# Kernel optimization log

Hardware: AMD Instinct MI355X
Metric: run time of the kernel (lower is better)

The kernel has to match this reference:

```python
import jax, jax.numpy as jnp
import numpy as np

B, N, H, T = 128, 512, 128, 32


def setup_inputs() -> dict:
    key = jax.random.key(0)
    ks = jax.random.split(key, 6)
    s = 0.05  # small init scale keeps softmax logits sane
    return {
        "encoder_outputs": jax.random.normal(ks[0], (B, N, H), jnp.float32),
        "W_ih": jax.random.normal(ks[1], (4 * H, H), jnp.float32) * s,
        "W_hh": jax.random.normal(ks[2], (4 * H, H), jnp.float32) * s,
        "b_ih": jnp.zeros((4 * H,), jnp.float32),
        "b_hh": jnp.zeros((4 * H,), jnp.float32),
        "W1": jax.random.normal(ks[3], (H, H), jnp.float32) * s,
        "W2": jax.random.normal(ks[4], (H, H), jnp.float32) * s,
        "v": jax.random.normal(ks[5], (H,), jnp.float32) * s,
        "decode_steps": T,
    }


def reference(encoder_outputs, W_ih, W_hh, b_ih, b_hh, W1, W2, v, decode_steps):
    b, n, h = encoder_outputs.shape
    dtype = encoder_outputs.dtype
    # W1(encoder_outputs) is loop-invariant: hoist it (same math as the torch loop)
    enc_trans = jnp.einsum("bnh,kh->bnk", encoder_outputs, W1)  # [B,n,H]

    dec0 = encoder_outputs.mean(axis=1)  # [B,H]
    hx0 = jnp.zeros((b, h), dtype)
    cx0 = jnp.zeros((b, h), dtype)
    mask0 = jnp.zeros((b, n), bool)
    key0 = jax.random.key(42)
    rows = jnp.arange(b)

    def step(carry, _):
        dec_input, hx, cx, mask, key = carry
        # torch.nn.LSTMCell: gates ordered i, f, g, o
        gates = dec_input @ W_ih.T + b_ih + hx @ W_hh.T + b_hh  # [B,4H]
        i, f, g, o = jnp.split(gates, 4, axis=-1)
        i = jax.nn.sigmoid(i)
        f = jax.nn.sigmoid(f)
        g = jnp.tanh(g)
        o = jax.nn.sigmoid(o)
        cx_new = f * cx + i * g
        hx_new = o * jnp.tanh(cx_new)
        # additive attention scores
        dec_trans = hx_new @ W2.T  # [B,H]
        scores = jnp.einsum("bnh,h->bn", jnp.tanh(enc_trans + dec_trans[:, None, :]), v)
        scores = jnp.where(mask, -jnp.inf, scores)  # masked_fill(-inf)
        # sample next node (torch.multinomial on softmax == categorical on logits)
        key, sub = jax.random.split(key)
        idx = jax.random.categorical(sub, scores, axis=-1)  # [B]
        probs = jax.nn.softmax(scores, axis=-1)
        sel_log_prob = jnp.log(jnp.take_along_axis(probs, idx[:, None], axis=1)[:, 0] + 1e-9)
        mask_new = mask.at[rows, idx].set(True)
        dec_next = jnp.take_along_axis(encoder_outputs, idx[:, None, None], axis=1)[:, 0]  # [B,H]
        return (dec_next, hx_new, cx_new, mask_new, key), (idx, sel_log_prob)

    _, (tours, log_probs) = jax.lax.scan(
        step, (dec0, hx0, cx0, mask0, key0), xs=None, length=decode_steps
    )
    return tours.T, log_probs.T  # [B,T], [B,T]
```

## Files before the change

### kernel.cpp

```cpp
#include <hip/hip_runtime.h>
#include <cstdint>
#include <cstddef>


constexpr int B = 128, N = 512, H = 128, T = 32;
constexpr int G4 = 4 * H;
constexpr float TINYF = 1.17549435e-38f;

__host__ __device__ inline uint32_t rotl32(uint32_t v, int d) {
  return (v << d) | (v >> (32 - d));
}

__host__ __device__ inline void tf2x32(uint32_t k0, uint32_t k1,
                                       uint32_t x0, uint32_t x1,
                                       uint32_t& o0, uint32_t& o1) {
  uint32_t ks2 = k0 ^ k1 ^ 0x1BD11BDAu;
  x0 += k0; x1 += k1;
#define TF_R(r) x0 += x1; x1 = rotl32(x1, (r)); x1 ^= x0;
  TF_R(13) TF_R(15) TF_R(26) TF_R(6)
  x0 += k1; x1 += ks2 + 1u;
  TF_R(17) TF_R(29) TF_R(16) TF_R(24)
  x0 += ks2; x1 += k0 + 2u;
  TF_R(13) TF_R(15) TF_R(26) TF_R(6)
  x0 += k0; x1 += k1 + 3u;
  TF_R(17) TF_R(29) TF_R(16) TF_R(24)
  x0 += k1; x1 += ks2 + 4u;
  TF_R(13) TF_R(15) TF_R(26) TF_R(6)
  x0 += ks2; x1 += k0 + 5u;
#undef TF_R
  o0 = x0; o1 = x1;
}

struct KeyArgs { uint32_t k[2 * T]; };

static KeyArgs make_subkeys() {
  KeyArgs ka;
  uint32_t k0 = 0u, k1 = 42u;
  for (int t = 0; t < T; ++t) {
    uint32_t n0, n1, s0, s1;
    tf2x32(k0, k1, 0u, 0u, n0, n1);
    tf2x32(k0, k1, 0u, 1u, s0, s1);
    ka.k[2 * t] = s0; ka.k[2 * t + 1] = s1;
    k0 = n0; k1 = n1;
  }
  return ka;
}

__device__ inline uint32_t gumbel_bits(uint32_t sk0, uint32_t sk1, int i) {
  uint32_t o0, o1;
  tf2x32(sk0, sk1, 0u, (uint32_t)i, o0, o1);
  return o0 ^ o1;
}

__device__ inline float fast_tanh(float x) {
  float cx = fminf(9.0f, fmaxf(-9.0f, x));
  float t = __expf(2.0f * cx);
  return (t - 1.0f) * __builtin_amdgcn_rcpf(t + 1.0f);
}

__global__ void k_transpose(const float* __restrict__ Wih, const float* __restrict__ Whh,
                            const float* __restrict__ W2, const float* __restrict__ W1,
                            float* __restrict__ WihT, float* __restrict__ WhhT,
                            float* __restrict__ W2T, float* __restrict__ W1T) {
  int i = blockIdx.x * blockDim.x + threadIdx.x;
  if (i < H * G4) {
    int h = i >> 9, j = i & (G4 - 1);
    WihT[i] = Wih[j * H + h];
  } else if (i < 2 * H * G4) {
    int q = i - H * G4; int h = q >> 9, j = q & (G4 - 1);
    WhhT[q] = Whh[j * H + h];
  } else if (i < 2 * H * G4 + H * H) {
    int q = i - 2 * H * G4; int h = q >> 7, k = q & (H - 1);
    W2T[q] = W2[k * H + h];
  } else if (i < 2 * H * G4 + 2 * H * H) {
    int q = i - 2 * H * G4 - H * H; int h = q >> 7, k = q & (H - 1);
    W1T[q] = W1[k * H + h];
  }
}

__global__ __launch_bounds__(256) void k_enc_trans(const float* __restrict__ enc,
                                                   const float* __restrict__ W1T,
                                                   float* __restrict__ encT2) {
  __shared__ __align__(16) float es[16 * 128];
  int blk = blockIdx.x;
  int b = blk >> 5;
  int n0 = (blk & 31) << 4;
  const float* src = enc + ((size_t)b * N + n0) * H;
  for (int i = threadIdx.x; i < 16 * 128; i += 256) es[i] = src[i];
  __syncthreads();
  int k = threadIdx.x & 127, ng = threadIdx.x >> 7;
  float acc[8] = {0.f, 0.f, 0.f, 0.f, 0.f, 0.f, 0.f, 0.f};
  for (int h = 0; h < H; h += 4) {
    float w0 = W1T[(h + 0) * H + k];
    float w1 = W1T[(h + 1) * H + k];
    float w2 = W1T[(h + 2) * H + k];
    float w3 = W1T[(h + 3) * H + k];
#pragma unroll
    for (int j = 0; j < 8; ++j) {
      const float4 e = *(const float4*)&es[(ng * 8 + j) * 128 + h];
      acc[j] += w0 * e.x + w1 * e.y + w2 * e.z + w3 * e.w;
    }
  }
  float* dst = encT2 + (size_t)b * H * N + (size_t)k * N + n0 + ng * 8;
  ((float4*)dst)[0] = make_float4(acc[0], acc[1], acc[2], acc[3]);
  ((float4*)dst)[1] = make_float4(acc[4], acc[5], acc[6], acc[7]);
}

__global__ __launch_bounds__(1024) void k_decode(
    const float* __restrict__ enc, const float* __restrict__ encT2,
    const float* __restrict__ WihT, const float* __restrict__ WhhT,
    const float* __restrict__ W2T,
    const float* __restrict__ bih, const float* __restrict__ bhh,
    const float* __restrict__ v,
    KeyArgs keys, float* __restrict__ out) {
  __shared__ __align__(16) float xs[H];
  __shared__ __align__(16) float hs[H];
  __shared__ __align__(16) float cs[H];
  __shared__ __align__(16) float dt[H];
  __shared__ __align__(16) float vv[H];
  __shared__ __align__(16) float bsum[G4];
  __shared__ float pg[2][G4];
  __shared__ float ps[2][N];
  __shared__ float pdt[4][H];
  __shared__ float sc[N];
  __shared__ float wr_z[8], wr_m[8], wr_s[8];
  __shared__ int wr_i[8];
  __shared__ float s_smax;
  __shared__ int s_idx;

  const int tid = threadIdx.x;
  const int b = blockIdx.x;
  const int lane = tid & 63;
  const int wave = tid >> 6;
  const int half = tid >> 9;
  const int id = tid & 511;

  if (tid < 512) {
    int h = tid & 127, part = tid >> 7;
    float s = 0.f;
    const float* p = enc + ((size_t)b * N + part * 128) * H + h;
#pragma unroll 8
    for (int n = 0; n < 128; ++n) s += p[(size_t)n * H];
    pdt[part][h] = s;
    bsum[tid] = bih[tid] + bhh[tid];
  }
  if (tid < 128) { hs[tid] = 0.f; cs[tid] = 0.f; vv[tid] = v[tid]; }
  __syncthreads();
  if (tid < 128)
    xs[tid] = (pdt[0][tid] + pdt[1][tid] + pdt[2][tid] + pdt[3][tid]) * (1.0f / N);
  bool masked = false;
  __syncthreads();

  for (int t = 0; t < T; ++t) {
    {
      const float* wi = WihT + (size_t)(half * 64) * G4 + id;
      const float* wh = WhhT + (size_t)(half * 64) * G4 + id;
      const int hb = half * 64;
      float a0 = 0.f, a1 = 0.f;
#pragma unroll 8
      for (int h = 0; h < 64; ++h) {
        a0 += wi[h * G4] * xs[hb + h];
        a1 += wh[h * G4] * hs[hb + h];
      }
      pg[half][id] = a0 + a1;
    }
    __syncthreads();
    if (tid < 128) {
      float gi = pg[0][tid] + pg[1][tid] + bsum[tid];
      float gf = pg[0][H + tid] + pg[1][H + tid] + bsum[H + tid];
      float gg = pg[0][2 * H + tid] + pg[1][2 * H + tid] + bsum[2 * H + tid];
      float go = pg[0][3 * H + tid] + pg[1][3 * H + tid] + bsum[3 * H + tid];
      gi = 1.0f / (1.0f + expf(-gi));
      gf = 1.0f / (1.0f + expf(-gf));
      gg = tanhf(gg);
      go = 1.0f / (1.0f + expf(-go));
      float c = gf * cs[tid] + gi * gg;
      cs[tid] = c;
      hs[tid] = go * tanhf(c);
    }
    __syncthreads();
    if (tid < 512) {
      int k = tid & 127, part = tid >> 7;
      const float* w2 = W2T + (size_t)(part * 32) * H + k;
      const int hb = part * 32;
      float a = 0.f;
#pragma unroll 8
      for (int h = 0; h < 32; ++h) a += w2[h * H] * hs[hb + h];
      pdt[part][k] = a;
    }
    __syncthreads();
    if (tid < 128) dt[tid] = pdt[0][tid] + pdt[1][tid] + pdt[2][tid] + pdt[3][tid];
    __syncthreads();
    {
      const int kb = half * 64;
      const float* ep = encT2 + (size_t)b * (H * N) + (size_t)kb * N + id;
      float a0 = 0.f, a1 = 0.f;
#pragma unroll 8
      for (int kk = 0; kk < 64; kk += 2) {
        float e0 = ep[(size_t)kk * N];
        float e1 = ep[(size_t)(kk + 1) * N];
        a0 += vv[kb + kk] * fast_tanh(e0 + dt[kb + kk]);
        a1 += vv[kb + kk + 1] * fast_tanh(e1 + dt[kb + kk + 1]);
      }
      ps[half][id] = a0 + a1;
    }
    __syncthreads();
    if (tid < 512) {
      float s = masked ? -INFINITY : (ps[0][tid] + ps[1][tid]);
      sc[tid] = s;
      uint32_t bits = gumbel_bits(keys.k[2 * t], keys.k[2 * t + 1], b * N + tid);
      float f = __uint_as_float((bits >> 9) | 0x3f800000u) - 1.0f;
      float u = fmaxf(TINYF, f + TINYF);
      float g = -logf(-logf(u));
      float z = s + g;
      int zi = tid;
      float m = s;
#pragma unroll
      for (int d = 32; d >= 1; d >>= 1) {
        float oz = __shfl_xor(z, d);
        int oi = __shfl_xor(zi, d);
        float om = __shfl_xor(m, d);
        if (oz > z || (oz == z && oi < zi)) { z = oz; zi = oi; }
        m = fmaxf(m, om);
      }
      if (lane == 0) { wr_z[wave] = z; wr_i[wave] = zi; wr_m[wave] = m; }
    }
    __syncthreads();
    if (tid == 0) {
      float bz = wr_z[0]; int bi = wr_i[0]; float bm = wr_m[0];
#pragma unroll
      for (int w = 1; w < 8; ++w) {
        if (wr_z[w] > bz || (wr_z[w] == bz && wr_i[w] < bi)) { bz = wr_z[w]; bi = wr_i[w]; }
        bm = fmaxf(bm, wr_m[w]);
      }
      s_idx = bi; s_smax = bm;
    }
    __syncthreads();
    if (tid < 512) {
      float e = expf(sc[tid] - s_smax);
#pragma unroll
      for (int d = 32; d >= 1; d >>= 1) e += __shfl_xor(e, d);
      if (lane == 0) wr_s[wave] = e;
      if (tid == s_idx) masked = true;
    } else if (tid < 640) {
      xs[tid - 512] = enc[((size_t)b * N + s_idx) * H + (tid - 512)];
    }
    __syncthreads();
    if (tid == 0) {
      float sum = wr_s[0] + wr_s[1] + wr_s[2] + wr_s[3]
                + wr_s[4] + wr_s[5] + wr_s[6] + wr_s[7];
      float p = expf(sc[s_idx] - s_smax) / sum;
      out[(size_t)b * T + t] = (float)s_idx;
      out[(size_t)B * T + (size_t)b * T + t] = logf(p + 1e-9f);
    }
    __syncthreads();
  }
}

extern "C" void kernel_launch(void* const* d_in, const int* in_sizes, int n_in,
                              void* d_out, int out_size, void* d_ws, size_t ws_size,
                              hipStream_t stream) {
  (void)in_sizes; (void)n_in; (void)out_size; (void)ws_size;
  const float* enc = (const float*)d_in[0];
  const float* Wih = (const float*)d_in[1];
  const float* Whh = (const float*)d_in[2];
  const float* bih = (const float*)d_in[3];
  const float* bhh = (const float*)d_in[4];
  const float* W1  = (const float*)d_in[5];
  const float* W2  = (const float*)d_in[6];
  const float* v   = (const float*)d_in[7];
  float* out = (float*)d_out;
  float* ws = (float*)d_ws;

  float* WihT  = ws;
  float* WhhT  = ws + 65536;
  float* W2T   = ws + 131072;
  float* W1T   = ws + 147456;
  float* encT2 = ws + 163840;

  KeyArgs keys = make_subkeys();

  k_transpose<<<640, 256, 0, stream>>>(Wih, Whh, W2, W1, WihT, WhhT, W2T, W1T);
  k_enc_trans<<<B * N / 16, 256, 0, stream>>>(enc, W1T, encT2);
  k_decode<<<B, 1024, 0, stream>>>(enc, encT2, WihT, WhhT, W2T, bih, bhh, v, keys, out);
}
```

Measured before the change: 615.0 us.

## Cache encoder projection in registers and stage W2/W_ih weights in LDS

Each thread loads its 64 elements of the transposed encoder projection into registers once, so the attention loop no longer re-reads them from global memory on every decode step. All of W2T and the first 32 rows of W_ihT are copied into 128KB of dynamic shared memory, and the gate and W2 matvecs read those weights from LDS. Shared-memory reads of the x, h, dt and v vectors are widened to float4. This needs many more VGPRs and most of the CU's LDS, so it risks register spills and requires raising the kernel's dynamic shared-memory limit.

```diff
diff --git a/kernel.cpp b/kernel.cpp
--- a/kernel.cpp
+++ b/kernel.cpp
@@ -128,6 +128,10 @@
   __shared__ float s_smax;
   __shared__ int s_idx;
 
+  extern __shared__ __align__(16) float dynlds[];
+  float* w2s = dynlds;
+  float* wis = dynlds + 16384;
+
   const int tid = threadIdx.x;
   const int b = blockIdx.x;
   const int lane = tid & 63;
@@ -135,6 +139,26 @@
   const int half = tid >> 9;
   const int id = tid & 511;
 
+  float er[64];
+  {
+    const int kb = half * 64;
+    const float* ep = encT2 + (size_t)b * (H * N) + (size_t)kb * N + id;
+#pragma unroll
+    for (int kk = 0; kk < 64; ++kk) er[kk] = ep[(size_t)kk * N];
+  }
+
+  {
+    const float4* s2 = (const float4*)W2T;
+    const float4* si = (const float4*)WihT;
+    float4* d2 = (float4*)w2s;
+    float4* di = (float4*)wis;
+#pragma unroll
+    for (int i = 0; i < 4; ++i) {
+      d2[tid + i * 1024] = s2[tid + i * 1024];
+      di[tid + i * 1024] = si[tid + i * 1024];
+    }
+  }
+
   if (tid < 512) {
     int h = tid & 127, part = tid >> 7;
     float s = 0.f;
@@ -153,14 +177,47 @@
 
   for (int t = 0; t < T; ++t) {
     {
-      const float* wi = WihT + (size_t)(half * 64) * G4 + id;
-      const float* wh = WhhT + (size_t)(half * 64) * G4 + id;
       const int hb = half * 64;
       float a0 = 0.f, a1 = 0.f;
-#pragma unroll 8
-      for (int h = 0; h < 64; ++h) {
-        a0 += wi[h * G4] * xs[hb + h];
-        a1 += wh[h * G4] * hs[hb + h];
+      if (half == 0) {
+#pragma unroll 8
+        for (int h = 0; h < 32; h += 4) {
+          const float4 xv = *(const float4*)&xs[h];
+          a0 += wis[(h + 0) * G4 + id] * xv.x;
+          a0 += wis[(h + 1) * G4 + id] * xv.y;
+          a0 += wis[(h + 2) * G4 + id] * xv.z;
+          a0 += wis[(h + 3) * G4 + id] * xv.w;
+        }
+        const float* wi = WihT + (size_t)32 * G4 + id;
+#pragma unroll 8
+        for (int h = 0; h < 32; h += 4) {
+          const float4 xv = *(const float4*)&xs[32 + h];
+          a0 += wi[(h + 0) * G4] * xv.x;
+          a0 += wi[(h + 1) * G4] * xv.y;
+          a0 += wi[(h + 2) * G4] * xv.z;
+          a0 += wi[(h + 3) * G4] * xv.w;
+        }
+      } else {
+        const float* wi = WihT + (size_t)64 * G4 + id;
+#pragma unroll 8
+        for (int h = 0; h < 64; h += 4) {
+          const float4 xv = *(const float4*)&xs[64 + h];
+          a0 += wi[(h + 0) * G4] * xv.x;
+          a0 += wi[(h + 1) * G4] * xv.y;
+          a0 += wi[(h + 2) * G4] * xv.z;
+          a0 += wi[(h + 3) * G4] * xv.w;
+        }
+      }
+      {
+        const float* wh = WhhT + (size_t)hb * G4 + id;
+#pragma unroll 8
+        for (int h = 0; h < 64; h += 4) {
+          const float4 hv = *(const float4*)&hs[hb + h];
+          a1 += wh[(h + 0) * G4] * hv.x;
+          a1 += wh[(h + 1) * G4] * hv.y;
+          a1 += wh[(h + 2) * G4] * hv.z;
+          a1 += wh[(h + 3) * G4] * hv.w;
+        }
       }
       pg[half][id] = a0 + a1;
     }
@@ -181,11 +238,16 @@
     __syncthreads();
     if (tid < 512) {
       int k = tid & 127, part = tid >> 7;
-      const float* w2 = W2T + (size_t)(part * 32) * H + k;
-      const int hb = part * 32;
+      const int hbp = part * 32;
       float a = 0.f;
 #pragma unroll 8
-      for (int h = 0; h < 32; ++h) a += w2[h * H] * hs[hb + h];
+      for (int h = 0; h < 32; h += 4) {
+        const float4 hv = *(const float4*)&hs[hbp + h];
+        a += w2s[(hbp + h + 0) * H + k] * hv.x;
+        a += w2s[(hbp + h + 1) * H + k] * hv.y;
+        a += w2s[(hbp + h + 2) * H + k] * hv.z;
+        a += w2s[(hbp + h + 3) * H + k] * hv.w;
+      }
       pdt[part][k] = a;
     }
     __syncthreads();
@@ -193,14 +255,15 @@
     __syncthreads();
     {
       const int kb = half * 64;
-      const float* ep = encT2 + (size_t)b * (H * N) + (size_t)kb * N + id;
       float a0 = 0.f, a1 = 0.f;
-#pragma unroll 8
-      for (int kk = 0; kk < 64; kk += 2) {
-        float e0 = ep[(size_t)kk * N];
-        float e1 = ep[(size_t)(kk + 1) * N];
-        a0 += vv[kb + kk] * fast_tanh(e0 + dt[kb + kk]);
-        a1 += vv[kb + kk + 1] * fast_tanh(e1 + dt[kb + kk + 1]);
+#pragma unroll
+      for (int k4 = 0; k4 < 64; k4 += 4) {
+        const float4 dv = *(const float4*)&dt[kb + k4];
+        const float4 vw = *(const float4*)&vv[kb + k4];
+        a0 += vw.x * fast_tanh(er[k4 + 0] + dv.x);
+        a1 += vw.y * fast_tanh(er[k4 + 1] + dv.y);
+        a0 += vw.z * fast_tanh(er[k4 + 2] + dv.z);
+        a1 += vw.w * fast_tanh(er[k4 + 3] + dv.w);
       }
       ps[half][id] = a0 + a1;
     }
@@ -280,7 +343,14 @@
 
   KeyArgs keys = make_subkeys();
 
+  static bool lds_attr_set = false;
+  if (!lds_attr_set) {
+    (void)hipFuncSetAttribute(reinterpret_cast<const void*>(k_decode),
+                              hipFuncAttributeMaxDynamicSharedMemorySize, 131072);
+    lds_attr_set = true;
+  }
+
   k_transpose<<<640, 256, 0, stream>>>(Wih, Whh, W2, W1, WihT, WhhT, W2T, W1T);
   k_enc_trans<<<B * N / 16, 256, 0, stream>>>(enc, W1T, encT2);
-  k_decode<<<B, 1024, 0, stream>>>(enc, encT2, WihT, WhhT, W2T, bih, bhh, v, keys, out);
-}
+  k_decode<<<B, 1024, 131072, stream>>>(enc, encT2, WihT, WhhT, W2T, bih, bhh, v, keys, out);
+}
```

Result: slower. 1.042 ms (+69.5%).

## Keep per-batch encoder transform resident in registers and LDS across decode steps

Applied to the files above, without the earlier changes.

The decode kernel now runs 512 threads per block instead of 1024. Each thread keeps 64 of its column's transformed encoder values in registers, and the other 64 rows (128 KB per batch) live in dynamic LDS. This removes the re-read of encT2 from global memory on every one of the 32 decode steps, and it removes the partial-sum shared buffers and one barrier. In exchange, threads per block are halved, so the LSTM gate matvec does twice the work per thread. The kernel also carries heavy register pressure and a large LDS allocation set via a function attribute.

```diff
diff --git a/kernel.cpp b/kernel.cpp
--- a/kernel.cpp
+++ b/kernel.cpp
@@ -106,7 +106,11 @@
   ((float4*)dst)[1] = make_float4(acc[4], acc[5], acc[6], acc[7]);
 }
 
-__global__ __launch_bounds__(1024) void k_decode(
+#define REP16(M) M(0) M(1) M(2) M(3) M(4) M(5) M(6) M(7) \
+                 M(8) M(9) M(10) M(11) M(12) M(13) M(14) M(15)
+
+__global__ __launch_bounds__(512)
+__attribute__((amdgpu_waves_per_eu(2, 2))) void k_decode(
     const float* __restrict__ enc, const float* __restrict__ encT2,
     const float* __restrict__ WihT, const float* __restrict__ WhhT,
     const float* __restrict__ W2T,
@@ -119,8 +123,7 @@
   __shared__ __align__(16) float dt[H];
   __shared__ __align__(16) float vv[H];
   __shared__ __align__(16) float bsum[G4];
-  __shared__ float pg[2][G4];
-  __shared__ float ps[2][N];
+  __shared__ float pg[G4];
   __shared__ float pdt[4][H];
   __shared__ float sc[N];
   __shared__ float wr_z[8], wr_m[8], wr_s[8];
@@ -128,14 +131,29 @@
   __shared__ float s_smax;
   __shared__ int s_idx;
 
+  extern __shared__ __align__(16) float e_lds[];
+
   const int tid = threadIdx.x;
   const int b = blockIdx.x;
   const int lane = tid & 63;
   const int wave = tid >> 6;
-  const int half = tid >> 9;
-  const int id = tid & 511;
-
-  if (tid < 512) {
+
+  const float* ep = encT2 + (size_t)b * (H * N) + tid;
+#define ERLD(i) float4 er##i = make_float4(ep[(size_t)(4*i+0) * N], \
+                                           ep[(size_t)(4*i+1) * N], \
+                                           ep[(size_t)(4*i+2) * N], \
+                                           ep[(size_t)(4*i+3) * N]);
+  REP16(ERLD)
+#undef ERLD
+
+  {
+    const float4* src4 = (const float4*)(encT2 + (size_t)b * (H * N) + (size_t)64 * N);
+    float4* dst4 = (float4*)e_lds;
+#pragma unroll
+    for (int i = 0; i < 16; ++i) dst4[tid + i * 512] = src4[tid + i * 512];
+  }
+
+  {
     int h = tid & 127, part = tid >> 7;
     float s = 0.f;
     const float* p = enc + ((size_t)b * N + part * 128) * H + h;
@@ -153,23 +171,43 @@
 
   for (int t = 0; t < T; ++t) {
     {
-      const float* wi = WihT + (size_t)(half * 64) * G4 + id;
-      const float* wh = WhhT + (size_t)(half * 64) * G4 + id;
-      const int hb = half * 64;
-      float a0 = 0.f, a1 = 0.f;
+      const float* wi = WihT + tid;
+      const float* wh = WhhT + tid;
+      float a0x = 0.f, a0h = 0.f, a1x = 0.f, a1h = 0.f;
 #pragma unroll 8
-      for (int h = 0; h < 64; ++h) {
-        a0 += wi[h * G4] * xs[hb + h];
-        a1 += wh[h * G4] * hs[hb + h];
-      }
-      pg[half][id] = a0 + a1;
+      for (int h = 0; h < 64; h += 4) {
+        const float4 xv = *(const float4*)&xs[h];
+        a0x += wi[(size_t)(h + 0) * G4] * xv.x;
+        a0x += wi[(size_t)(h + 1) * G4] * xv.y;
+        a0x += wi[(size_t)(h + 2) * G4] * xv.z;
+        a0x += wi[(size_t)(h + 3) * G4] * xv.w;
+        const float4 hv = *(const float4*)&hs[h];
+        a0h += wh[(size_t)(h + 0) * G4] * hv.x;
+        a0h += wh[(size_t)(h + 1) * G4] * hv.y;
+        a0h += wh[(size_t)(h + 2) * G4] * hv.z;
+        a0h += wh[(size_t)(h + 3) * G4] * hv.w;
+      }
+#pragma unroll 8
+      for (int h = 64; h < 128; h += 4) {
+        const float4 xv = *(const float4*)&xs[h];
+        a1x += wi[(size_t)(h + 0) * G4] * xv.x;
+        a1x += wi[(size_t)(h + 1) * G4] * xv.y;
+        a1x += wi[(size_t)(h + 2) * G4] * xv.z;
+        a1x += wi[(size_t)(h + 3) * G4] * xv.w;
+        const float4 hv = *(const float4*)&hs[h];
+        a1h += wh[(size_t)(h + 0) * G4] * hv.x;
+        a1h += wh[(size_t)(h + 1) * G4] * hv.y;
+        a1h += wh[(size_t)(h + 2) * G4] * hv.z;
+        a1h += wh[(size_t)(h + 3) * G4] * hv.w;
+      }
+      pg[tid] = (a0x + a0h) + (a1x + a1h);
     }
     __syncthreads();
     if (tid < 128) {
-      float gi = pg[0][tid] + pg[1][tid] + bsum[tid];
-      float gf = pg[0][H + tid] + pg[1][H + tid] + bsum[H + tid];
-      float gg = pg[0][2 * H + tid] + pg[1][2 * H + tid] + bsum[2 * H + tid];
-      float go = pg[0][3 * H + tid] + pg[1][3 * H + tid] + bsum[3 * H + tid];
+      float gi = pg[tid] + bsum[tid];
+      float gf = pg[H + tid] + bsum[H + tid];
+      float gg = pg[2 * H + tid] + bsum[2 * H + tid];
+      float go = pg[3 * H + tid] + bsum[3 * H + tid];
       gi = 1.0f / (1.0f + expf(-gi));
       gf = 1.0f / (1.0f + expf(-gf));
       gg = tanhf(gg);
@@ -179,35 +217,54 @@
       hs[tid] = go * tanhf(c);
     }
     __syncthreads();
-    if (tid < 512) {
+    {
       int k = tid & 127, part = tid >> 7;
       const float* w2 = W2T + (size_t)(part * 32) * H + k;
-      const int hb = part * 32;
+      const int hbp = part * 32;
       float a = 0.f;
 #pragma unroll 8
-      for (int h = 0; h < 32; ++h) a += w2[h * H] * hs[hb + h];
+      for (int h = 0; h < 32; h += 4) {
+        const float4 hv = *(const float4*)&hs[hbp + h];
+        a += w2[(size_t)(h + 0) * H] * hv.x;
+        a += w2[(size_t)(h + 1) * H] * hv.y;
+        a += w2[(size_t)(h + 2) * H] * hv.z;
+        a += w2[(size_t)(h + 3) * H] * hv.w;
+      }
       pdt[part][k] = a;
     }
     __syncthreads();
     if (tid < 128) dt[tid] = pdt[0][tid] + pdt[1][tid] + pdt[2][tid] + pdt[3][tid];
     __syncthreads();
-    {
-      const int kb = half * 64;
-      const float* ep = encT2 + (size_t)b * (H * N) + (size_t)kb * N + id;
+    float s_score;
+    {
       float a0 = 0.f, a1 = 0.f;
-#pragma unroll 8
-      for (int kk = 0; kk < 64; kk += 2) {
-        float e0 = ep[(size_t)kk * N];
-        float e1 = ep[(size_t)(kk + 1) * N];
-        a0 += vv[kb + kk] * fast_tanh(e0 + dt[kb + kk]);
-        a1 += vv[kb + kk + 1] * fast_tanh(e1 + dt[kb + kk + 1]);
-      }
-      ps[half][id] = a0 + a1;
-    }
-    __syncthreads();
-    if (tid < 512) {
-      float s = masked ? -INFINITY : (ps[0][tid] + ps[1][tid]);
-      sc[tid] = s;
+#define P4A(i) { const float4 dv = *(const float4*)&dt[4 * i];              \
+                 const float4 vw = *(const float4*)&vv[4 * i];              \
+                 a0 += vw.x * fast_tanh(er##i.x + dv.x);                    \
+                 a1 += vw.y * fast_tanh(er##i.y + dv.y);                    \
+                 a0 += vw.z * fast_tanh(er##i.z + dv.z);                    \
+                 a1 += vw.w * fast_tanh(er##i.w + dv.w); }
+      REP16(P4A)
+#undef P4A
+      float b0 = 0.f, b1 = 0.f;
+#pragma unroll
+      for (int k4 = 0; k4 < 64; k4 += 4) {
+        const float e0 = e_lds[(k4 + 0) * N + tid];
+        const float e1 = e_lds[(k4 + 1) * N + tid];
+        const float e2 = e_lds[(k4 + 2) * N + tid];
+        const float e3 = e_lds[(k4 + 3) * N + tid];
+        const float4 dv = *(const float4*)&dt[64 + k4];
+        const float4 vw = *(const float4*)&vv[64 + k4];
+        b0 += vw.x * fast_tanh(e0 + dv.x);
+        b1 += vw.y * fast_tanh(e1 + dv.y);
+        b0 += vw.z * fast_tanh(e2 + dv.z);
+        b1 += vw.w * fast_tanh(e3 + dv.w);
+      }
+      s_score = (a0 + a1) + (b0 + b1);
+    }
+    float s = masked ? -INFINITY : s_score;
+    sc[tid] = s;
+    {
       uint32_t bits = gumbel_bits(keys.k[2 * t], keys.k[2 * t + 1], b * N + tid);
       float f = __uint_as_float((bits >> 9) | 0x3f800000u) - 1.0f;
       float u = fmaxf(TINYF, f + TINYF);
@@ -236,14 +293,15 @@
       s_idx = bi; s_smax = bm;
     }
     __syncthreads();
-    if (tid < 512) {
-      float e = expf(sc[tid] - s_smax);
+    {
+      float xnew = 0.f;
+      if (tid < 128) xnew = enc[((size_t)b * N + s_idx) * H + tid];
+      float e = expf(s - s_smax);
 #pragma unroll
       for (int d = 32; d >= 1; d >>= 1) e += __shfl_xor(e, d);
       if (lane == 0) wr_s[wave] = e;
       if (tid == s_idx) masked = true;
-    } else if (tid < 640) {
-      xs[tid - 512] = enc[((size_t)b * N + s_idx) * H + (tid - 512)];
+      if (tid < 128) xs[tid] = xnew;
     }
     __syncthreads();
     if (tid == 0) {
@@ -280,7 +338,14 @@
 
   KeyArgs keys = make_subkeys();
 
+  static bool lds_attr_set = false;
+  if (!lds_attr_set) {
+    (void)hipFuncSetAttribute(reinterpret_cast<const void*>(k_decode),
+                              hipFuncAttributeMaxDynamicSharedMemorySize, 131072);
+    lds_attr_set = true;
+  }
+
   k_transpose<<<640, 256, 0, stream>>>(Wih, Whh, W2, W1, WihT, WhhT, W2T, W1T);
   k_enc_trans<<<B * N / 16, 256, 0, stream>>>(enc, W1T, encT2);
-  k_decode<<<B, 1024, 0, stream>>>(enc, encT2, WihT, WhhT, W2T, bih, bhh, v, keys, out);
-}
+  k_decode<<<B, 512, 131072, stream>>>(enc, encT2, WihT, WhhT, W2T, bih, bhh, v, keys, out);
+}
```

After: 590.3 us. 1.04x faster.

## Process two batch rows per block and stage part of encT2 in LDS

Applied to the files above, without the earlier changes.

Each 1024-thread block now handles two batch rows, one per 512-thread half, so the decode kernel launches B/2 blocks. The LSTM gate and W2 matvecs load each weight once and apply it to both rows' hidden states, halving weight traffic per row. The first 32 of the 128 k-slices of the per-row transformed encoder tile are copied into 128KB of dynamic LDS before the loop, and the score loop reads those from LDS while the rest still come from global memory. The trade-offs are half as many blocks (64 CUs busy), a large LDS allocation, and gate work done by only 512 threads per step.

```diff
diff --git a/kernel.cpp b/kernel.cpp
--- a/kernel.cpp
+++ b/kernel.cpp
@@ -113,107 +113,196 @@
     const float* __restrict__ bih, const float* __restrict__ bhh,
     const float* __restrict__ v,
     KeyArgs keys, float* __restrict__ out) {
-  __shared__ __align__(16) float xs[H];
-  __shared__ __align__(16) float hs[H];
-  __shared__ __align__(16) float cs[H];
-  __shared__ __align__(16) float dt[H];
+  __shared__ __align__(16) float xs[2][H];
+  __shared__ __align__(16) float hs[2][H];
+  __shared__ __align__(16) float cs[2][H];
+  __shared__ __align__(16) float dt[2][H];
   __shared__ __align__(16) float vv[H];
   __shared__ __align__(16) float bsum[G4];
   __shared__ float pg[2][G4];
-  __shared__ float ps[2][N];
-  __shared__ float pdt[4][H];
-  __shared__ float sc[N];
-  __shared__ float wr_z[8], wr_m[8], wr_s[8];
-  __shared__ int wr_i[8];
-  __shared__ float s_smax;
-  __shared__ int s_idx;
+  __shared__ float pdt[2][4][H];
+  __shared__ float sc[2][N];
+  __shared__ float wr_z[2][8], wr_m[2][8], wr_s[2][8];
+  __shared__ int wr_i[2][8];
+  __shared__ float s_smax[2];
+  __shared__ int s_idx[2];
+
+  extern __shared__ __align__(16) float e_lds[];
 
   const int tid = threadIdx.x;
-  const int b = blockIdx.x;
-  const int lane = tid & 63;
-  const int wave = tid >> 6;
   const int half = tid >> 9;
   const int id = tid & 511;
-
-  if (tid < 512) {
-    int h = tid & 127, part = tid >> 7;
+  const int lane = tid & 63;
+  const int wv = (tid >> 6) & 7;
+  const int b = blockIdx.x + 64 * half;
+
+  {
+    const float4* src4 = (const float4*)(encT2 + (size_t)b * (H * N));
+    float4* dst4 = (float4*)e_lds + (size_t)half * 4096;
+#pragma unroll
+    for (int i = 0; i < 8; ++i) dst4[id + i * 512] = src4[id + i * 512];
+  }
+
+  {
+    int h = tid & 127, part = (tid >> 7) & 3;
     float s = 0.f;
     const float* p = enc + ((size_t)b * N + part * 128) * H + h;
 #pragma unroll 8
     for (int n = 0; n < 128; ++n) s += p[(size_t)n * H];
-    pdt[part][h] = s;
-    bsum[tid] = bih[tid] + bhh[tid];
-  }
-  if (tid < 128) { hs[tid] = 0.f; cs[tid] = 0.f; vv[tid] = v[tid]; }
+    pdt[half][part][h] = s;
+  }
+  if (tid < 512) bsum[tid] = bih[tid] + bhh[tid];
+  if (id < 128) { hs[half][id] = 0.f; cs[half][id] = 0.f; }
+  if (tid < 128) vv[tid] = v[tid];
   __syncthreads();
-  if (tid < 128)
-    xs[tid] = (pdt[0][tid] + pdt[1][tid] + pdt[2][tid] + pdt[3][tid]) * (1.0f / N);
+  if (id < 128)
+    xs[half][id] = (pdt[half][0][id] + pdt[half][1][id] +
+                    pdt[half][2][id] + pdt[half][3][id]) * (1.0f / N);
   bool masked = false;
   __syncthreads();
 
   for (int t = 0; t < T; ++t) {
-    {
-      const float* wi = WihT + (size_t)(half * 64) * G4 + id;
-      const float* wh = WhhT + (size_t)(half * 64) * G4 + id;
-      const int hb = half * 64;
-      float a0 = 0.f, a1 = 0.f;
-#pragma unroll 8
-      for (int h = 0; h < 64; ++h) {
-        a0 += wi[h * G4] * xs[hb + h];
-        a1 += wh[h * G4] * hs[hb + h];
-      }
-      pg[half][id] = a0 + a1;
-    }
-    __syncthreads();
-    if (tid < 128) {
-      float gi = pg[0][tid] + pg[1][tid] + bsum[tid];
-      float gf = pg[0][H + tid] + pg[1][H + tid] + bsum[H + tid];
-      float gg = pg[0][2 * H + tid] + pg[1][2 * H + tid] + bsum[2 * H + tid];
-      float go = pg[0][3 * H + tid] + pg[1][3 * H + tid] + bsum[3 * H + tid];
+    if (tid < 512) {
+      const float* wi = WihT + tid;
+      const float* wh = WhhT + tid;
+      float a0x0 = 0.f, a0h0 = 0.f, a1x0 = 0.f, a1h0 = 0.f;
+      float a0x1 = 0.f, a0h1 = 0.f, a1x1 = 0.f, a1h1 = 0.f;
+#pragma unroll 4
+      for (int h = 0; h < 64; h += 4) {
+        const float w0 = wi[(size_t)(h + 0) * G4];
+        const float w1 = wi[(size_t)(h + 1) * G4];
+        const float w2 = wi[(size_t)(h + 2) * G4];
+        const float w3 = wi[(size_t)(h + 3) * G4];
+        const float4 x0 = *(const float4*)&xs[0][h];
+        const float4 x1 = *(const float4*)&xs[1][h];
+        a0x0 += w0 * x0.x; a0x0 += w1 * x0.y; a0x0 += w2 * x0.z; a0x0 += w3 * x0.w;
+        a0x1 += w0 * x1.x; a0x1 += w1 * x1.y; a0x1 += w2 * x1.z; a0x1 += w3 * x1.w;
+        const float u0 = wh[(size_t)(h + 0) * G4];
+        const float u1 = wh[(size_t)(h + 1) * G4];
+        const float u2 = wh[(size_t)(h + 2) * G4];
+        const float u3 = wh[(size_t)(h + 3) * G4];
+        const float4 h0 = *(const float4*)&hs[0][h];
+        const float4 h1 = *(const float4*)&hs[1][h];
+        a0h0 += u0 * h0.x; a0h0 += u1 * h0.y; a0h0 += u2 * h0.z; a0h0 += u3 * h0.w;
+        a0h1 += u0 * h1.x; a0h1 += u1 * h1.y; a0h1 += u2 * h1.z; a0h1 += u3 * h1.w;
+      }
+#pragma unroll 4
+      for (int h = 64; h < 128; h += 4) {
+        const float w0 = wi[(size_t)(h + 0) * G4];
+        const float w1 = wi[(size_t)(h + 1) * G4];
+        const float w2 = wi[(size_t)(h + 2) * G4];
+        const float w3 = wi[(size_t)(h + 3) * G4];
+        const float4 x0 = *(const float4*)&xs[0][h];
+        const float4 x1 = *(const float4*)&xs[1][h];
+        a1x0 += w0 * x0.x; a1x0 += w1 * x0.y; a1x0 += w2 * x0.z; a1x0 += w3 * x0.w;
+        a1x1 += w0 * x1.x; a1x1 += w1 * x1.y; a1x1 += w2 * x1.z; a1x1 += w3 * x1.w;
+        const float u0 = wh[(size_t)(h + 0) * G4];
+        const float u1 = wh[(size_t)(h + 1) * G4];
+        const float u2 = wh[(size_t)(h + 2) * G4];
+        const float u3 = wh[(size_t)(h + 3) * G4];
+        const float4 h0 = *(const float4*)&hs[0][h];
+        const float4 h1 = *(const float4*)&hs[1][h];
+        a1h0 += u0 * h0.x; a1h0 += u1 * h0.y; a1h0 += u2 * h0.z; a1h0 += u3 * h0.w;
+        a1h1 += u0 * h1.x; a1h1 += u1 * h1.y; a1h1 += u2 * h1.z; a1h1 += u3 * h1.w;
+      }
+      pg[0][tid] = (a0x0 + a0h0) + (a1x0 + a1h0);
+      pg[1][tid] = (a0x1 + a0h1) + (a1x1 + a1h1);
+    }
+    __syncthreads();
+    if (id < 128) {
+      float gi = pg[half][id] + bsum[id];
+      float gf = pg[half][H + id] + bsum[H + id];
+      float gg = pg[half][2 * H + id] + bsum[2 * H + id];
+      float go = pg[half][3 * H + id] + bsum[3 * H + id];
       gi = 1.0f / (1.0f + expf(-gi));
       gf = 1.0f / (1.0f + expf(-gf));
       gg = tanhf(gg);
       go = 1.0f / (1.0f + expf(-go));
-      float c = gf * cs[tid] + gi * gg;
-      cs[tid] = c;
-      hs[tid] = go * tanhf(c);
+      float c = gf * cs[half][id] + gi * gg;
+      cs[half][id] = c;
+      hs[half][id] = go * tanhf(c);
     }
     __syncthreads();
     if (tid < 512) {
       int k = tid & 127, part = tid >> 7;
       const float* w2 = W2T + (size_t)(part * 32) * H + k;
-      const int hb = part * 32;
-      float a = 0.f;
-#pragma unroll 8
-      for (int h = 0; h < 32; ++h) a += w2[h * H] * hs[hb + h];
-      pdt[part][k] = a;
-    }
-    __syncthreads();
-    if (tid < 128) dt[tid] = pdt[0][tid] + pdt[1][tid] + pdt[2][tid] + pdt[3][tid];
-    __syncthreads();
+      const int hbp = part * 32;
+      float a0 = 0.f, a1 = 0.f;
+#pragma unroll 4
+      for (int h = 0; h < 32; h += 4) {
+        const float w0 = w2[(size_t)(h + 0) * H];
+        const float w1 = w2[(size_t)(h + 1) * H];
+        const float w2v = w2[(size_t)(h + 2) * H];
+        const float w3 = w2[(size_t)(h + 3) * H];
+        const float4 h0 = *(const float4*)&hs[0][hbp + h];
+        const float4 h1 = *(const float4*)&hs[1][hbp + h];
+        a0 += w0 * h0.x; a0 += w1 * h0.y; a0 += w2v * h0.z; a0 += w3 * h0.w;
+        a1 += w0 * h1.x; a1 += w1 * h1.y; a1 += w2v * h1.z; a1 += w3 * h1.w;
+      }
+      pdt[0][part][k] = a0;
+      pdt[1][part][k] = a1;
+    }
+    __syncthreads();
+    if (id < 128)
+      dt[half][id] = pdt[half][0][id] + pdt[half][1][id] +
+                     pdt[half][2][id] + pdt[half][3][id];
+    __syncthreads();
+    float s_score;
     {
-      const int kb = half * 64;
-      const float* ep = encT2 + (size_t)b * (H * N) + (size_t)kb * N + id;
+      const float* eg = encT2 + (size_t)b * (H * N) + id;
+      const float* el = e_lds + (size_t)half * 16384 + id;
       float a0 = 0.f, a1 = 0.f;
-#pragma unroll 8
-      for (int kk = 0; kk < 64; kk += 2) {
-        float e0 = ep[(size_t)kk * N];
-        float e1 = ep[(size_t)(kk + 1) * N];
-        a0 += vv[kb + kk] * fast_tanh(e0 + dt[kb + kk]);
-        a1 += vv[kb + kk + 1] * fast_tanh(e1 + dt[kb + kk + 1]);
-      }
-      ps[half][id] = a0 + a1;
-    }
-    __syncthreads();
-    if (tid < 512) {
-      float s = masked ? -INFINITY : (ps[0][tid] + ps[1][tid]);
-      sc[tid] = s;
-      uint32_t bits = gumbel_bits(keys.k[2 * t], keys.k[2 * t + 1], b * N + tid);
+#pragma unroll
+      for (int k4 = 0; k4 < 32; k4 += 4) {
+        const float e0 = el[(k4 + 0) * 512];
+        const float e1 = el[(k4 + 1) * 512];
+        const float e2 = el[(k4 + 2) * 512];
+        const float e3 = el[(k4 + 3) * 512];
+        const float4 dv = *(const float4*)&dt[half][k4];
+        const float4 vw = *(const float4*)&vv[k4];
+        a0 += vw.x * fast_tanh(e0 + dv.x);
+        a1 += vw.y * fast_tanh(e1 + dv.y);
+        a0 += vw.z * fast_tanh(e2 + dv.z);
+        a1 += vw.w * fast_tanh(e3 + dv.w);
+      }
+#pragma unroll 4
+      for (int k4 = 32; k4 < 64; k4 += 4) {
+        const float e0 = eg[(size_t)(k4 + 0) * N];
+        const float e1 = eg[(size_t)(k4 + 1) * N];
+        const float e2 = eg[(size_t)(k4 + 2) * N];
+        const float e3 = eg[(size_t)(k4 + 3) * N];
+        const float4 dv = *(const float4*)&dt[half][k4];
+        const float4 vw = *(const float4*)&vv[k4];
+        a0 += vw.x * fast_tanh(e0 + dv.x);
+        a1 += vw.y * fast_tanh(e1 + dv.y);
+        a0 += vw.z * fast_tanh(e2 + dv.z);
+        a1 += vw.w * fast_tanh(e3 + dv.w);
+      }
+      float b0 = 0.f, b1 = 0.f;
+#pragma unroll 4
+      for (int k4 = 64; k4 < 128; k4 += 4) {
+        const float e0 = eg[(size_t)(k4 + 0) * N];
+        const float e1 = eg[(size_t)(k4 + 1) * N];
+        const float e2 = eg[(size_t)(k4 + 2) * N];
+        const float e3 = eg[(size_t)(k4 + 3) * N];
+        const float4 dv = *(const float4*)&dt[half][k4];
+        const float4 vw = *(const float4*)&vv[k4];
+        b0 += vw.x * fast_tanh(e0 + dv.x);
+        b1 += vw.y * fast_tanh(e1 + dv.y);
+        b0 += vw.z * fast_tanh(e2 + dv.z);
+        b1 += vw.w * fast_tanh(e3 + dv.w);
+      }
+      s_score = (a0 + a1) + (b0 + b1);
+    }
+    float s = masked ? -INFINITY : s_score;
+    sc[half][id] = s;
+    {
+      uint32_t bits = gumbel_bits(keys.k[2 * t], keys.k[2 * t + 1], b * N + id);
       float f = __uint_as_float((bits >> 9) | 0x3f800000u) - 1.0f;
       float u = fmaxf(TINYF, f + TINYF);
       float g = -logf(-logf(u));
       float z = s + g;
-      int zi = tid;
+      int zi = id;
       float m = s;
 #pragma unroll
       for (int d = 32; d >= 1; d >>= 1) {
@@ -223,34 +312,37 @@
         if (oz > z || (oz == z && oi < zi)) { z = oz; zi = oi; }
         m = fmaxf(m, om);
       }
-      if (lane == 0) { wr_z[wave] = z; wr_i[wave] = zi; wr_m[wave] = m; }
-    }
-    __syncthreads();
-    if (tid == 0) {
-      float bz = wr_z[0]; int bi = wr_i[0]; float bm = wr_m[0];
+      if (lane == 0) { wr_z[half][wv] = z; wr_i[half][wv] = zi; wr_m[half][wv] = m; }
+    }
+    __syncthreads();
+    if (id == 0) {
+      float bz = wr_z[half][0]; int bi = wr_i[half][0]; float bm = wr_m[half][0];
 #pragma unroll
       for (int w = 1; w < 8; ++w) {
-        if (wr_z[w] > bz || (wr_z[w] == bz && wr_i[w] < bi)) { bz = wr_z[w]; bi = wr_i[w]; }
-        bm = fmaxf(bm, wr_m[w]);
-      }
-      s_idx = bi; s_smax = bm;
-    }
-    __syncthreads();
-    if (tid < 512) {
-      float e = expf(sc[tid] - s_smax);
+        if (wr_z[half][w] > bz || (wr_z[half][w] == bz && wr_i[half][w] < bi)) {
+          bz = wr_z[half][w]; bi = wr_i[half][w];
+        }
+        bm = fmaxf(bm, wr_m[half][w]);
+      }
+      s_idx[half] = bi; s_smax[half] = bm;
+    }
+    __syncthreads();
+    {
+      float xnew = 0.f;
+      if (id < 128) xnew = enc[((size_t)b * N + s_idx[half]) * H + id];
+      float e = expf(s - s_smax[half]);
 #pragma unroll
       for (int d = 32; d >= 1; d >>= 1) e += __shfl_xor(e, d);
-      if (lane == 0) wr_s[wave] = e;
-      if (tid == s_idx) masked = true;
-    } else if (tid < 640) {
-      xs[tid - 512] = enc[((size_t)b * N + s_idx) * H + (tid - 512)];
-    }
-    __syncthreads();
-    if (tid == 0) {
-      float sum = wr_s[0] + wr_s[1] + wr_s[2] + wr_s[3]
-                + wr_s[4] + wr_s[5] + wr_s[6] + wr_s[7];
-      float p = expf(sc[s_idx] - s_smax) / sum;
-      out[(size_t)b * T + t] = (float)s_idx;
+      if (lane == 0) wr_s[half][wv] = e;
+      if (id == s_idx[half]) masked = true;
+      if (id < 128) xs[half][id] = xnew;
+    }
+    __syncthreads();
+    if (id == 0) {
+      float sum = wr_s[half][0] + wr_s[half][1] + wr_s[half][2] + wr_s[half][3]
+                + wr_s[half][4] + wr_s[half][5] + wr_s[half][6] + wr_s[half][7];
+      float p = expf(sc[half][s_idx[half]] - s_smax[half]) / sum;
+      out[(size_t)b * T + t] = (float)s_idx[half];
       out[(size_t)B * T + (size_t)b * T + t] = logf(p + 1e-9f);
     }
     __syncthreads();
@@ -280,7 +372,15 @@
 
   KeyArgs keys = make_subkeys();
 
+  static bool lds_attr_set = false;
+  if (!lds_attr_set) {
+    (void)hipFuncSetAttribute(reinterpret_cast<const void*>(k_decode),
+                              hipFuncAttributeMaxDynamicSharedMemorySize, 131072);
+    lds_attr_set = true;
+  }
+
   k_transpose<<<640, 256, 0, stream>>>(Wih, Whh, W2, W1, WihT, WhhT, W2T, W1T);
   k_enc_trans<<<B * N / 16, 256, 0, stream>>>(enc, W1T, encT2);
-  k_decode<<<B, 1024, 0, stream>>>(enc, encT2, WihT, WhhT, W2T, bih, bhh, v, keys, out);
-}
+  k_decode<<<B / 2, 1024, 131072, stream>>>(enc, encT2, WihT, WhhT, W2T,
+                                            bih, bhh, v, keys, out);
+}
```

Result: slower. 853.5 us (+38.8%).
